# Kernel tuning notes

Hardware: AMD Instinct MI355X
Metric: run time of the kernel (lower is better)

The kernel has to match this reference:

```python
import jax, jax.numpy as jnp
import numpy as np


def setup_inputs() -> dict:
    key = jax.random.key(0)
    k1, k2, k3, k4 = jax.random.split(key, 4)
    N, F, E = 131072, 512, 256
    x = jax.random.normal(k1, (N, F), dtype=jnp.float32)
    W = jax.random.normal(k2, (E, F), dtype=jnp.float32) * 0.05  # stacked weak-classifier weights
    b = jax.random.normal(k3, (E,), dtype=jnp.float32) * 0.05
    alphas = jax.random.normal(k4, (E,), dtype=jnp.float32)
    return {"x": x, "W": W, "b": b, "alphas": alphas}


def reference(x, W, b, alphas):
    # Fused version of the per-estimator Python loop:
    # per estimator e: pred_e = round(sigmoid(x @ W[e] + b[e])) in {0,1}
    logits = jnp.einsum('nf,ef->ne', x, W) + b              # [N, E]
    preds = jnp.round(jax.nn.sigmoid(logits))               # [N, E], half-to-even like torch.round
    # original casts each (alpha * pred) term to long (trunc toward zero) before accumulating
    terms = jnp.trunc(alphas[None, :] * preds)              # [N, E]
    acc = jnp.sum(terms, axis=1)                            # [N]
    return jnp.sign(acc)
```

## Files before the change

### kernel.cpp

```cpp
#include <hip/hip_runtime.h>
#include <math.h>


#define F_DIM 512
#define E_DIM 256
#define BMROWS 128
#define CPP    96
#define NTMAX  6
#define NSLOT  288
#define TAU    1e-3f

typedef float f32x4  __attribute__((ext_vector_type(4)));
typedef short bf16x8 __attribute__((ext_vector_type(8)));

__device__ inline unsigned short bf16_rne(float v) {
    unsigned u = __float_as_uint(v);
    u += 0x7FFFu + ((u >> 16) & 1u);
    return (unsigned short)(u >> 16);
}
__device__ inline float bf16_to_f32(unsigned short h) {
    return __uint_as_float(((unsigned)h) << 16);
}
__device__ inline void cvt8(const float4& a, const float4& b, bf16x8& h8, bf16x8& l8) {
    const float v[8] = {a.x, a.y, a.z, a.w, b.x, b.y, b.z, b.w};
    #pragma unroll
    for (int j = 0; j < 8; ++j) {
        const unsigned short h = bf16_rne(v[j]);
        h8[j] = (short)h;
        l8[j] = (short)bf16_rne(v[j] - bf16_to_f32(h));
    }
}

__device__ __attribute__((noinline)) bool exact_pred(const float* __restrict__ xr,
                                                     const float* __restrict__ wr,
                                                     float bv) {
    double s0 = 0.0, s1 = 0.0, s2 = 0.0, s3 = 0.0;
    for (int k = 0; k < F_DIM; k += 4) {
        s0 = fma((double)xr[k + 0], (double)wr[k + 0], s0);
        s1 = fma((double)xr[k + 1], (double)wr[k + 1], s1);
        s2 = fma((double)xr[k + 2], (double)wr[k + 2], s2);
        s3 = fma((double)xr[k + 3], (double)wr[k + 3], s3);
    }
    double s = ((s0 + s1) + (s2 + s3)) + (double)bv;
    return s > 0.0;
}

__global__ __launch_bounds__(1024)
void ada_prep(const float* __restrict__ W, const float* __restrict__ alphas,
              unsigned short* __restrict__ whi, unsigned short* __restrict__ wlo) {
    __shared__ int se[NSLOT];
    __shared__ int wcnt[16];

    const int tid = threadIdx.x;
    if (tid < NSLOT) se[tid] = -1;
    if (tid < 16) wcnt[tid] = 0;
    __syncthreads();

    const bool in_e = (tid < E_DIM);
    const float t = in_e ? truncf(alphas[tid]) : 0.0f;
    const bool flag = in_e && (t != 0.0f);
    const unsigned long long m64 = __ballot(flag);
    const int lane = tid & 63, wvi = tid >> 6;
    if (lane == 0) wcnt[wvi] = __popcll(m64);
    __syncthreads();
    if (flag) {
        int off = 0;
        #pragma unroll
        for (int w = 0; w < 4; ++w) if (w < wvi) off += wcnt[w];
        se[off + __popcll(m64 & ((1ull << lane) - 1ull))] = tid;
    }
    __syncthreads();

    for (int p = tid; p < NSLOT * (F_DIM / 2); p += 1024) {
        const int row = p >> 8;
        const int cp  = (p & 255) * 2;
        const int e   = se[row];
        float2 v = make_float2(0.0f, 0.0f);
        if (e >= 0) v = *(const float2*)(W + (size_t)e * F_DIM + cp);
        ushort2 h2, l2;
        h2.x = bf16_rne(v.x); l2.x = bf16_rne(v.x - bf16_to_f32(h2.x));
        h2.y = bf16_rne(v.y); l2.y = bf16_rne(v.y - bf16_to_f32(h2.y));
        *(ushort2*)(whi + (size_t)row * F_DIM + cp) = h2;
        *(ushort2*)(wlo + (size_t)row * F_DIM + cp) = l2;
    }
}

template<bool PREW>
__global__ __launch_bounds__(256)
void ada_gemm(const float* __restrict__ x, const float* __restrict__ W,
              const float* __restrict__ bias, const float* __restrict__ alphas,
              const unsigned short* __restrict__ whi,
              const unsigned short* __restrict__ wlo,
              float* __restrict__ out) {
    __shared__ int   se[NSLOT];
    __shared__ float st[NSLOT];
    __shared__ float sb[NSLOT];
    __shared__ int   wcnt[4];

    const int tid = threadIdx.x;

    se[tid] = 0; st[tid] = 0.0f; sb[tid] = 0.0f;
    if (tid < NSLOT - E_DIM) { se[E_DIM + tid] = 0; st[E_DIM + tid] = 0.0f; sb[E_DIM + tid] = 0.0f; }
    __syncthreads();
    const float t = truncf(alphas[tid]);
    const bool flag = (t != 0.0f);
    const unsigned long long m64 = __ballot(flag);
    const int lane = tid & 63, wvi = tid >> 6;
    if (lane == 0) wcnt[wvi] = __popcll(m64);
    __syncthreads();
    const int M = wcnt[0] + wcnt[1] + wcnt[2] + wcnt[3];
    if (flag) {
        int off = 0;
        #pragma unroll
        for (int w = 0; w < 4; ++w) if (w < wvi) off += wcnt[w];
        const int slot = off + __popcll(m64 & ((1ull << lane) - 1ull));
        se[slot] = tid; st[slot] = t; sb[slot] = bias[tid];
    }
    __syncthreads();

    const int l15  = tid & 15;
    const int quad = (tid >> 4) & 3;
    const int wave = tid >> 6;
    const int rowbase = blockIdx.x * BMROWS + wave * 32;
    const float* xrow = x + (size_t)(rowbase + l15) * F_DIM + quad * 8;

    int part[2][4];
    #pragma unroll
    for (int mt = 0; mt < 2; ++mt)
        #pragma unroll
        for (int r = 0; r < 4; ++r) part[mt][r] = 0;

    for (int cb = 0; cb < M; cb += CPP) {
        const int Mrem = M - cb;
        const int NT = ((Mrem + 15) >> 4) < NTMAX ? ((Mrem + 15) >> 4) : NTMAX;

        f32x4 acc[2][NTMAX];
        #pragma unroll
        for (int mt = 0; mt < 2; ++mt)
            #pragma unroll
            for (int nt = 0; nt < NTMAX; ++nt)
                acc[mt][nt] = (f32x4){0.0f, 0.0f, 0.0f, 0.0f};

        const unsigned short* bhp[NTMAX];
        const unsigned short* blp[NTMAX];
        const float* wrp[NTMAX];
        #pragma unroll
        for (int nt = 0; nt < NTMAX; ++nt) {
            const int col = cb + nt * 16 + l15;
            if (PREW) {
                bhp[nt] = whi + (size_t)col * F_DIM + quad * 8;
                blp[nt] = wlo + (size_t)col * F_DIM + quad * 8;
            } else {
                wrp[nt] = W + (size_t)se[col] * F_DIM + quad * 8;
            }
        }

        float4 xc0[2], xc1[2];
        #pragma unroll
        for (int mt = 0; mt < 2; ++mt) {
            const float* p = xrow + (size_t)mt * 16 * F_DIM;
            xc0[mt] = *(const float4*)(p);
            xc1[mt] = *(const float4*)(p + 4);
        }

        for (int k0 = 0; k0 < F_DIM; k0 += 32) {
            float4 xn0[2], xn1[2];
            const bool more = (k0 + 32) < F_DIM;
            if (more) {
                #pragma unroll
                for (int mt = 0; mt < 2; ++mt) {
                    const float* p = xrow + (size_t)mt * 16 * F_DIM + k0 + 32;
                    xn0[mt] = *(const float4*)(p);
                    xn1[mt] = *(const float4*)(p + 4);
                }
            }

            bf16x8 ah[2], al[2];
            #pragma unroll
            for (int mt = 0; mt < 2; ++mt)
                cvt8(xc0[mt], xc1[mt], ah[mt], al[mt]);

            #pragma unroll
            for (int nt = 0; nt < NTMAX; ++nt) {
                if (nt < NT) {
                    bf16x8 bh, bl;
                    if (PREW) {
                        bh = *(const bf16x8*)(bhp[nt] + k0);
                        bl = *(const bf16x8*)(blp[nt] + k0);
                    } else {
                        const float4 wa = *(const float4*)(wrp[nt] + k0);
                        const float4 wb = *(const float4*)(wrp[nt] + k0 + 4);
                        cvt8(wa, wb, bh, bl);
                    }
                    #pragma unroll
                    for (int mt = 0; mt < 2; ++mt) {
                        acc[mt][nt] = __builtin_amdgcn_mfma_f32_16x16x32_bf16(ah[mt], bh, acc[mt][nt], 0, 0, 0);
                        acc[mt][nt] = __builtin_amdgcn_mfma_f32_16x16x32_bf16(al[mt], bh, acc[mt][nt], 0, 0, 0);
                        acc[mt][nt] = __builtin_amdgcn_mfma_f32_16x16x32_bf16(ah[mt], bl, acc[mt][nt], 0, 0, 0);
                    }
                }
            }

            if (more) {
                #pragma unroll
                for (int mt = 0; mt < 2; ++mt) { xc0[mt] = xn0[mt]; xc1[mt] = xn1[mt]; }
            }
        }

        #pragma unroll
        for (int nt = 0; nt < NTMAX; ++nt) {
            if (nt < NT) {
                const int col = cb + nt * 16 + l15;
                const float tv = st[col];
                if (tv != 0.0f) {
                    const float bv = sb[col];
                    const int it = (int)tv;
                    #pragma unroll
                    for (int mt = 0; mt < 2; ++mt) {
                        #pragma unroll
                        for (int r = 0; r < 4; ++r) {
                            const float logit = acc[mt][nt][r] + bv;
                            bool pred = (logit > 0.0f);
                            if (fabsf(logit) < TAU) {
                                const int grow = rowbase + mt * 16 + quad * 4 + r;
                                pred = exact_pred(x + (size_t)grow * F_DIM,
                                                  W + (size_t)se[col] * F_DIM, bv);
                            }
                            if (pred) part[mt][r] += it;
                        }
                    }
                }
            }
        }
    }

    #pragma unroll
    for (int mt = 0; mt < 2; ++mt) {
        #pragma unroll
        for (int r = 0; r < 4; ++r) {
            int v = part[mt][r];
            v += __shfl_xor(v, 1);
            v += __shfl_xor(v, 2);
            v += __shfl_xor(v, 4);
            v += __shfl_xor(v, 8);
            part[mt][r] = v;
        }
    }
    if (l15 == 0) {
        #pragma unroll
        for (int mt = 0; mt < 2; ++mt) {
            float4 o;
            o.x = (part[mt][0] > 0) ? 1.0f : (part[mt][0] < 0 ? -1.0f : 0.0f);
            o.y = (part[mt][1] > 0) ? 1.0f : (part[mt][1] < 0 ? -1.0f : 0.0f);
            o.z = (part[mt][2] > 0) ? 1.0f : (part[mt][2] < 0 ? -1.0f : 0.0f);
            o.w = (part[mt][3] > 0) ? 1.0f : (part[mt][3] < 0 ? -1.0f : 0.0f);
            *(float4*)(out + rowbase + mt * 16 + quad * 4) = o;
        }
    }
}

extern "C" void kernel_launch(void* const* d_in, const int* in_sizes, int n_in,
                              void* d_out, int out_size, void* d_ws, size_t ws_size,
                              hipStream_t stream) {
    const float* x      = (const float*)d_in[0];
    const float* W      = (const float*)d_in[1];
    const float* bias   = (const float*)d_in[2];
    const float* alphas = (const float*)d_in[3];
    float* out = (float*)d_out;

    const int n = in_sizes[0] / F_DIM;
    const int nblocks = n / BMROWS;

    const size_t wsneed = (size_t)NSLOT * F_DIM * 2 * sizeof(unsigned short);
    if (ws_size >= wsneed) {
        unsigned short* whi = (unsigned short*)d_ws;
        unsigned short* wlo = whi + (size_t)NSLOT * F_DIM;
        ada_prep<<<dim3(1), dim3(1024), 0, stream>>>(W, alphas, whi, wlo);
        ada_gemm<true><<<dim3(nblocks), dim3(256), 0, stream>>>(x, W, bias, alphas, whi, wlo, out);
    } else {
        ada_gemm<false><<<dim3(nblocks), dim3(256), 0, stream>>>(x, W, bias, alphas, nullptr, nullptr, out);
    }
}
```

Baseline: 567.4 us.

## Defer near-zero logit exact checks to separate fixup kernel via global list

Instead of running the double-precision exact dot product inline inside the GEMM epilogue when a logit is within tolerance of zero, the GEMM now appends (row, estimator) pairs to a global list through an atomic counter. A separate fixup kernel recomputes those cases exactly and atomically adds to the output, then a sign kernel finalizes. The weight prep kernel is also spread across one block per slot instead of a single block. This removes divergent, register-heavy inline exact paths from the GEMM, at the cost of extra launches, global atomics and a list buffer.

```diff
diff --git a/kernel.cpp b/kernel.cpp
--- a/kernel.cpp
+++ b/kernel.cpp
@@ -13,15 +13,15 @@
 typedef float f32x4  __attribute__((ext_vector_type(4)));
 typedef short bf16x8 __attribute__((ext_vector_type(8)));
 
-__device__ inline unsigned short bf16_rne(float v) {
+__device__ __forceinline__ unsigned short bf16_rne(float v) {
     unsigned u = __float_as_uint(v);
     u += 0x7FFFu + ((u >> 16) & 1u);
     return (unsigned short)(u >> 16);
 }
-__device__ inline float bf16_to_f32(unsigned short h) {
+__device__ __forceinline__ float bf16_to_f32(unsigned short h) {
     return __uint_as_float(((unsigned)h) << 16);
 }
-__device__ inline void cvt8(const float4& a, const float4& b, bf16x8& h8, bf16x8& l8) {
+__device__ __forceinline__ void cvt8(const float4& a, const float4& b, bf16x8& h8, bf16x8& l8) {
     const float v[8] = {a.x, a.y, a.z, a.w, b.x, b.y, b.z, b.w};
     #pragma unroll
     for (int j = 0; j < 8; ++j) {
@@ -31,9 +31,9 @@
     }
 }
 
-__device__ __attribute__((noinline)) bool exact_pred(const float* __restrict__ xr,
-                                                     const float* __restrict__ wr,
-                                                     float bv) {
+__device__ __forceinline__ bool exact_pred(const float* __restrict__ xr,
+                                           const float* __restrict__ wr,
+                                           float bv) {
     double s0 = 0.0, s1 = 0.0, s2 = 0.0, s3 = 0.0;
     for (int k = 0; k < F_DIM; k += 4) {
         s0 = fma((double)xr[k + 0], (double)wr[k + 0], s0);
@@ -45,52 +45,49 @@
     return s > 0.0;
 }
 
-__global__ __launch_bounds__(1024)
+__global__ __launch_bounds__(256)
 void ada_prep(const float* __restrict__ W, const float* __restrict__ alphas,
-              unsigned short* __restrict__ whi, unsigned short* __restrict__ wlo) {
-    __shared__ int se[NSLOT];
-    __shared__ int wcnt[16];
-
-    const int tid = threadIdx.x;
-    if (tid < NSLOT) se[tid] = -1;
-    if (tid < 16) wcnt[tid] = 0;
-    __syncthreads();
-
-    const bool in_e = (tid < E_DIM);
-    const float t = in_e ? truncf(alphas[tid]) : 0.0f;
-    const bool flag = in_e && (t != 0.0f);
+              unsigned short* __restrict__ whi, unsigned short* __restrict__ wlo,
+              int* __restrict__ counter) {
+    __shared__ int wcnt[4];
+    __shared__ int slot_e;
+
+    const int tid  = threadIdx.x;
+    const int slot = blockIdx.x;
+    if (slot == 0 && tid == 0) *counter = 0;
+
+    const float t = truncf(alphas[tid]);
+    const bool flag = (t != 0.0f);
     const unsigned long long m64 = __ballot(flag);
     const int lane = tid & 63, wvi = tid >> 6;
     if (lane == 0) wcnt[wvi] = __popcll(m64);
+    if (tid == 0) slot_e = -1;
     __syncthreads();
     if (flag) {
         int off = 0;
         #pragma unroll
         for (int w = 0; w < 4; ++w) if (w < wvi) off += wcnt[w];
-        se[off + __popcll(m64 & ((1ull << lane) - 1ull))] = tid;
-    }
-    __syncthreads();
-
-    for (int p = tid; p < NSLOT * (F_DIM / 2); p += 1024) {
-        const int row = p >> 8;
-        const int cp  = (p & 255) * 2;
-        const int e   = se[row];
-        float2 v = make_float2(0.0f, 0.0f);
-        if (e >= 0) v = *(const float2*)(W + (size_t)e * F_DIM + cp);
-        ushort2 h2, l2;
-        h2.x = bf16_rne(v.x); l2.x = bf16_rne(v.x - bf16_to_f32(h2.x));
-        h2.y = bf16_rne(v.y); l2.y = bf16_rne(v.y - bf16_to_f32(h2.y));
-        *(ushort2*)(whi + (size_t)row * F_DIM + cp) = h2;
-        *(ushort2*)(wlo + (size_t)row * F_DIM + cp) = l2;
-    }
-}
-
-template<bool PREW>
+        if (off + __popcll(m64 & ((1ull << lane) - 1ull)) == slot) slot_e = tid;
+    }
+    __syncthreads();
+
+    const int e = slot_e;
+    const int cp = tid * 2;
+    float2 v = make_float2(0.0f, 0.0f);
+    if (e >= 0) v = *(const float2*)(W + (size_t)e * F_DIM + cp);
+    ushort2 h2, l2;
+    h2.x = bf16_rne(v.x); l2.x = bf16_rne(v.x - bf16_to_f32(h2.x));
+    h2.y = bf16_rne(v.y); l2.y = bf16_rne(v.y - bf16_to_f32(h2.y));
+    *(ushort2*)(whi + (size_t)slot * F_DIM + cp) = h2;
+    *(ushort2*)(wlo + (size_t)slot * F_DIM + cp) = l2;
+}
+
 __global__ __launch_bounds__(256)
-void ada_gemm(const float* __restrict__ x, const float* __restrict__ W,
-              const float* __restrict__ bias, const float* __restrict__ alphas,
+void ada_gemm(const float* __restrict__ x,
+              const float* __restrict__ alphas, const float* __restrict__ bias,
               const unsigned short* __restrict__ whi,
               const unsigned short* __restrict__ wlo,
+              int* __restrict__ counter, int2* __restrict__ list, int cap,
               float* __restrict__ out) {
     __shared__ int   se[NSLOT];
     __shared__ float st[NSLOT];
@@ -143,16 +140,11 @@
 
         const unsigned short* bhp[NTMAX];
         const unsigned short* blp[NTMAX];
-        const float* wrp[NTMAX];
         #pragma unroll
         for (int nt = 0; nt < NTMAX; ++nt) {
             const int col = cb + nt * 16 + l15;
-            if (PREW) {
-                bhp[nt] = whi + (size_t)col * F_DIM + quad * 8;
-                blp[nt] = wlo + (size_t)col * F_DIM + quad * 8;
-            } else {
-                wrp[nt] = W + (size_t)se[col] * F_DIM + quad * 8;
-            }
+            bhp[nt] = whi + (size_t)col * F_DIM + quad * 8;
+            blp[nt] = wlo + (size_t)col * F_DIM + quad * 8;
         }
 
         float4 xc0[2], xc1[2];
@@ -183,15 +175,8 @@
             #pragma unroll
             for (int nt = 0; nt < NTMAX; ++nt) {
                 if (nt < NT) {
-                    bf16x8 bh, bl;
-                    if (PREW) {
-                        bh = *(const bf16x8*)(bhp[nt] + k0);
-                        bl = *(const bf16x8*)(blp[nt] + k0);
-                    } else {
-                        const float4 wa = *(const float4*)(wrp[nt] + k0);
-                        const float4 wb = *(const float4*)(wrp[nt] + k0 + 4);
-                        cvt8(wa, wb, bh, bl);
-                    }
+                    const bf16x8 bh = *(const bf16x8*)(bhp[nt] + k0);
+                    const bf16x8 bl = *(const bf16x8*)(blp[nt] + k0);
                     #pragma unroll
                     for (int mt = 0; mt < 2; ++mt) {
                         acc[mt][nt] = __builtin_amdgcn_mfma_f32_16x16x32_bf16(ah[mt], bh, acc[mt][nt], 0, 0, 0);
@@ -204,6 +189,170 @@
             if (more) {
                 #pragma unroll
                 for (int mt = 0; mt < 2; ++mt) { xc0[mt] = xn0[mt]; xc1[mt] = xn1[mt]; }
+            }
+        }
+
+        #pragma unroll
+        for (int nt = 0; nt < NTMAX; ++nt) {
+            if (nt < NT) {
+                const int col = cb + nt * 16 + l15;
+                const float tv = st[col];
+                if (tv != 0.0f) {
+                    const float bv = sb[col];
+                    const int it = (int)tv;
+                    #pragma unroll
+                    for (int mt = 0; mt < 2; ++mt) {
+                        #pragma unroll
+                        for (int r = 0; r < 4; ++r) {
+                            const float logit = acc[mt][nt][r] + bv;
+                            if (fabsf(logit) >= TAU) {
+                                if (logit > 0.0f) part[mt][r] += it;
+                            } else {
+                                const int grow = rowbase + mt * 16 + quad * 4 + r;
+                                const int idx = atomicAdd(counter, 1);
+                                if (idx < cap) {
+                                    list[idx] = make_int2(grow, se[col] | (it << 16));
+                                } else if (logit > 0.0f) {
+                                    part[mt][r] += it;
+                                }
+                            }
+                        }
+                    }
+                }
+            }
+        }
+    }
+
+    #pragma unroll
+    for (int mt = 0; mt < 2; ++mt) {
+        #pragma unroll
+        for (int r = 0; r < 4; ++r) {
+            int v = part[mt][r];
+            v += __shfl_xor(v, 1);
+            v += __shfl_xor(v, 2);
+            v += __shfl_xor(v, 4);
+            v += __shfl_xor(v, 8);
+            part[mt][r] = v;
+        }
+    }
+    if (l15 == 0) {
+        #pragma unroll
+        for (int mt = 0; mt < 2; ++mt) {
+            float4 o;
+            o.x = (float)part[mt][0];
+            o.y = (float)part[mt][1];
+            o.z = (float)part[mt][2];
+            o.w = (float)part[mt][3];
+            *(float4*)(out + rowbase + mt * 16 + quad * 4) = o;
+        }
+    }
+}
+
+__global__ __launch_bounds__(256)
+void ada_fixup(const float* __restrict__ x, const float* __restrict__ W,
+               const float* __restrict__ bias,
+               const int* __restrict__ counter, const int2* __restrict__ list,
+               int cap, float* __restrict__ out) {
+    int n = *counter;
+    if (n > cap) n = cap;
+    const int stride = gridDim.x * blockDim.x;
+    for (int i = blockIdx.x * blockDim.x + threadIdx.x; i < n; i += stride) {
+        const int2 ent = list[i];
+        const int row = ent.x;
+        const int e   = ent.y & 0xFFFF;
+        const int it  = ent.y >> 16;
+        if (exact_pred(x + (size_t)row * F_DIM, W + (size_t)e * F_DIM, bias[e]))
+            atomicAdd(out + row, (float)it);
+    }
+}
+
+__global__ __launch_bounds__(256)
+void ada_sign(float* __restrict__ out) {
+    const int i = (blockIdx.x * blockDim.x + threadIdx.x) * 4;
+    float4 v = *(float4*)(out + i);
+    v.x = (v.x > 0.0f) ? 1.0f : (v.x < 0.0f ? -1.0f : 0.0f);
+    v.y = (v.y > 0.0f) ? 1.0f : (v.y < 0.0f ? -1.0f : 0.0f);
+    v.z = (v.z > 0.0f) ? 1.0f : (v.z < 0.0f ? -1.0f : 0.0f);
+    v.w = (v.w > 0.0f) ? 1.0f : (v.w < 0.0f ? -1.0f : 0.0f);
+    *(float4*)(out + i) = v;
+}
+
+__global__ __launch_bounds__(256)
+void ada_gemm_fb(const float* __restrict__ x, const float* __restrict__ W,
+                 const float* __restrict__ bias, const float* __restrict__ alphas,
+                 float* __restrict__ out) {
+    __shared__ int   se[NSLOT];
+    __shared__ float st[NSLOT];
+    __shared__ float sb[NSLOT];
+    __shared__ int   wcnt[4];
+
+    const int tid = threadIdx.x;
+    se[tid] = 0; st[tid] = 0.0f; sb[tid] = 0.0f;
+    if (tid < NSLOT - E_DIM) { se[E_DIM + tid] = 0; st[E_DIM + tid] = 0.0f; sb[E_DIM + tid] = 0.0f; }
+    __syncthreads();
+    const float t = truncf(alphas[tid]);
+    const bool flag = (t != 0.0f);
+    const unsigned long long m64 = __ballot(flag);
+    const int lane = tid & 63, wvi = tid >> 6;
+    if (lane == 0) wcnt[wvi] = __popcll(m64);
+    __syncthreads();
+    const int M = wcnt[0] + wcnt[1] + wcnt[2] + wcnt[3];
+    if (flag) {
+        int off = 0;
+        #pragma unroll
+        for (int w = 0; w < 4; ++w) if (w < wvi) off += wcnt[w];
+        const int slot = off + __popcll(m64 & ((1ull << lane) - 1ull));
+        se[slot] = tid; st[slot] = t; sb[slot] = bias[tid];
+    }
+    __syncthreads();
+
+    const int l15  = tid & 15;
+    const int quad = (tid >> 4) & 3;
+    const int wave = tid >> 6;
+    const int rowbase = blockIdx.x * BMROWS + wave * 32;
+    const float* xrow = x + (size_t)(rowbase + l15) * F_DIM + quad * 8;
+
+    int part[2][4];
+    #pragma unroll
+    for (int mt = 0; mt < 2; ++mt)
+        #pragma unroll
+        for (int r = 0; r < 4; ++r) part[mt][r] = 0;
+
+    for (int cb = 0; cb < M; cb += CPP) {
+        const int Mrem = M - cb;
+        const int NT = ((Mrem + 15) >> 4) < NTMAX ? ((Mrem + 15) >> 4) : NTMAX;
+
+        f32x4 acc[2][NTMAX];
+        #pragma unroll
+        for (int mt = 0; mt < 2; ++mt)
+            #pragma unroll
+            for (int nt = 0; nt < NTMAX; ++nt)
+                acc[mt][nt] = (f32x4){0.0f, 0.0f, 0.0f, 0.0f};
+
+        const float* wrp[NTMAX];
+        #pragma unroll
+        for (int nt = 0; nt < NTMAX; ++nt)
+            wrp[nt] = W + (size_t)se[cb + nt * 16 + l15] * F_DIM + quad * 8;
+
+        for (int k0 = 0; k0 < F_DIM; k0 += 32) {
+            bf16x8 ah[2], al[2];
+            #pragma unroll
+            for (int mt = 0; mt < 2; ++mt) {
+                const float* p = xrow + (size_t)mt * 16 * F_DIM + k0;
+                cvt8(*(const float4*)(p), *(const float4*)(p + 4), ah[mt], al[mt]);
+            }
+            #pragma unroll
+            for (int nt = 0; nt < NTMAX; ++nt) {
+                if (nt < NT) {
+                    bf16x8 bh, bl;
+                    cvt8(*(const float4*)(wrp[nt] + k0), *(const float4*)(wrp[nt] + k0 + 4), bh, bl);
+                    #pragma unroll
+                    for (int mt = 0; mt < 2; ++mt) {
+                        acc[mt][nt] = __builtin_amdgcn_mfma_f32_16x16x32_bf16(ah[mt], bh, acc[mt][nt], 0, 0, 0);
+                        acc[mt][nt] = __builtin_amdgcn_mfma_f32_16x16x32_bf16(al[mt], bh, acc[mt][nt], 0, 0, 0);
+                        acc[mt][nt] = __builtin_amdgcn_mfma_f32_16x16x32_bf16(ah[mt], bl, acc[mt][nt], 0, 0, 0);
+                    }
+                }
             }
         }
 
@@ -271,13 +420,24 @@
     const int n = in_sizes[0] / F_DIM;
     const int nblocks = n / BMROWS;
 
-    const size_t wsneed = (size_t)NSLOT * F_DIM * 2 * sizeof(unsigned short);
-    if (ws_size >= wsneed) {
-        unsigned short* whi = (unsigned short*)d_ws;
-        unsigned short* wlo = whi + (size_t)NSLOT * F_DIM;
-        ada_prep<<<dim3(1), dim3(1024), 0, stream>>>(W, alphas, whi, wlo);
-        ada_gemm<true><<<dim3(nblocks), dim3(256), 0, stream>>>(x, W, bias, alphas, whi, wlo, out);
+    const size_t whl_bytes = (size_t)NSLOT * F_DIM * sizeof(unsigned short);
+    const size_t fixed     = 64 + 2 * whl_bytes;
+    const long long cap_ll = ((long long)ws_size - (long long)fixed) / (long long)sizeof(int2);
+
+    if (cap_ll >= 4096) {
+        char* p = (char*)d_ws;
+        int*            counter = (int*)p;
+        unsigned short* whi     = (unsigned short*)(p + 64);
+        unsigned short* wlo     = (unsigned short*)(p + 64 + whl_bytes);
+        int2*           list    = (int2*)(p + fixed);
+        const int cap = (int)(cap_ll > 2000000 ? 2000000 : cap_ll);
+
+        ada_prep<<<dim3(NSLOT), dim3(256), 0, stream>>>(W, alphas, whi, wlo, counter);
+        ada_gemm<<<dim3(nblocks), dim3(256), 0, stream>>>(x, alphas, bias, whi, wlo,
+                                                          counter, list, cap, out);
+        ada_fixup<<<dim3(64), dim3(256), 0, stream>>>(x, W, bias, counter, list, cap, out);
+        ada_sign<<<dim3(n / 1024), dim3(256), 0, stream>>>(out);
     } else {
-        ada_gemm<false><<<dim3(nblocks), dim3(256), 0, stream>>>(x, W, bias, alphas, nullptr, nullptr, out);
-    }
-}
+        ada_gemm_fb<<<dim3(nblocks), dim3(256), 0, stream>>>(x, W, bias, alphas, out);
+    }
+}
```

Measured after the change: 517.7 us. 1.1x faster.
